# Optimization experiments

Measured on AMD Instinct MI355X. Metric: run time of the kernel, lower is better.

The kernel has to match this reference:

```python
import jax, jax.numpy as jnp
import numpy as np

B, S, D, H, DFF = 4, 2048, 1024, 16, 4096
DH = D // H  # per-head query/value dim
EPS = 1e-5


def layer_norm(x, scale, bias):
    mu = jnp.mean(x, axis=-1, keepdims=True)
    var = jnp.mean(jnp.square(x - mu), axis=-1, keepdims=True)
    return (x - mu) * jax.lax.rsqrt(var + EPS) * scale + bias


def setup_inputs() -> dict:
    key = jax.random.key(0)
    ks = jax.random.split(key, 16)
    s_in = 1.0 / np.sqrt(D)
    s_ff = 1.0 / np.sqrt(DFF)
    inp = {
        "x": jax.random.normal(ks[0], (B, S, D), jnp.float32),
        # per-head Q/K/V projections stacked along head axis [H, D, DH]
        "wq": jax.random.normal(ks[1], (H, D, DH), jnp.float32) * s_in,
        "bq": jax.random.normal(ks[2], (H, DH), jnp.float32) * 0.01,
        "wk": jax.random.normal(ks[3], (H, D, DH), jnp.float32) * s_in,
        "bk": jax.random.normal(ks[4], (H, DH), jnp.float32) * 0.01,
        "wv": jax.random.normal(ks[5], (H, D, DH), jnp.float32) * s_in,
        "bv": jax.random.normal(ks[6], (H, DH), jnp.float32) * 0.01,
        "wo": jax.random.normal(ks[7], (H * DH, D), jnp.float32) * s_in,
        "bo": jax.random.normal(ks[8], (D,), jnp.float32) * 0.01,
        "ln1_s": jnp.ones((D,), jnp.float32),
        "ln1_b": jnp.zeros((D,), jnp.float32),
        "w1": jax.random.normal(ks[9], (D, DFF), jnp.float32) * s_in,
        "b1": jax.random.normal(ks[10], (DFF,), jnp.float32) * 0.01,
        "w2": jax.random.normal(ks[11], (DFF, D), jnp.float32) * s_ff,
        "b2": jax.random.normal(ks[12], (D,), jnp.float32) * 0.01,
        "ln2_s": jnp.ones((D,), jnp.float32),
        "ln2_b": jnp.zeros((D,), jnp.float32),
    }
    return inp


def reference(x, wq, bq, wk, bk, wv, bv, wo, bo, ln1_s, ln1_b, w1, b1, w2, b2, ln2_s, ln2_b):
    # --- masked multi-head self-attention (all heads vectorized) ---
    q = jnp.einsum('bsd,hde->bhse', x, wq) + bq[None, :, None, :]  # [B,H,S,DH]
    k = jnp.einsum('bsd,hde->bhse', x, wk) + bk[None, :, None, :]
    v = jnp.einsum('bsd,hde->bhse', x, wv) + bv[None, :, None, :]
    scores = jnp.einsum('bhse,bhte->bhst', q, k)  # [B,H,S,S]
    causal = jnp.tril(jnp.ones((S, S), bool))  # mask sets strict upper triangle to -inf
    scores = jnp.where(causal, scores, -jnp.inf)
    scale = jnp.float32(DH) ** 0.5
    attn = jax.nn.softmax(scores / scale, axis=-1)
    out = jnp.einsum('bhst,bhte->bhse', attn, v)  # [B,H,S,DH]
    concat = out.transpose(0, 2, 1, 3).reshape(B, S, H * DH)
    attn_out = concat @ wo + bo
    y = layer_norm(x + attn_out, ln1_s, ln1_b)  # post-LN residual (dropout=0)
    # --- feed-forward ---
    ff = jax.nn.relu(y @ w1 + b1) @ w2 + b2
    return layer_norm(y + ff, ln2_s, ln2_b)
```

## Files before the change

kernel.cpp:

```cpp
#include <hip/hip_runtime.h>
#include <hip/hip_bf16.h>
#include <cstdint>

#define BB 4
#define SS 2048
#define DD 1024
#define HH 16
#define DHH 64
#define DFFN 4096
#define MROWS (BB*SS)

typedef __attribute__((ext_vector_type(8))) __bf16 v8bf;
typedef __attribute__((ext_vector_type(4))) float v4f;

static __device__ __forceinline__ unsigned short f2bf(float f) {
  unsigned u = __float_as_uint(f);
  u = (u + 0x7fffu + ((u >> 16) & 1u)) >> 16;
  return (unsigned short)u;
}

static __device__ __forceinline__ unsigned bf2bits(__hip_bfloat162 h) {
  union { __hip_bfloat162 h; unsigned u; } cv; cv.h = h; return cv.u;
}

static __device__ __forceinline__ void mfma16(v4f& d, v8bf a, v8bf b) {
  d = __builtin_amdgcn_mfma_f32_16x16x32_bf16(a, b, d, 0, 0, 0);
}

static __device__ __forceinline__ void gload16(const void* g, void* l) {
  __builtin_amdgcn_global_load_lds(
      (const __attribute__((address_space(1))) unsigned int*)(unsigned long long)g,
      (__attribute__((address_space(3))) unsigned int*)(unsigned int)(unsigned long long)l,
      16, 0, 0);
}

static __device__ __forceinline__ unsigned xcd_work(unsigned hw, unsigned nwg) {
  return (hw & 7u) * (nwg >> 3) + (hw >> 3);
}


__global__ __launch_bounds__(256) void pack_x_k(const float* __restrict__ x,
                                                unsigned short* __restrict__ xb) {
  int i = blockIdx.x * 256 + threadIdx.x;
  float4 v = ((const float4*)x)[i];
  ushort4 o;
  o.x = f2bf(v.x); o.y = f2bf(v.y); o.z = f2bf(v.z); o.w = f2bf(v.w);
  ((ushort4*)xb)[i] = o;
}

static __device__ __forceinline__ void transpose_tile(const float* __restrict__ src,
                                                      unsigned short* __restrict__ dst,
                                                      int R, int C, int rt, int ct) {
  __shared__ float tile[32][33];
  const int tx = threadIdx.x, ty = threadIdx.y;
  #pragma unroll
  for (int j = 0; j < 4; ++j)
    tile[ty + j * 8][tx] = src[(size_t)(rt + ty + j * 8) * C + ct + tx];
  __syncthreads();
  #pragma unroll
  for (int j = 0; j < 4; ++j)
    dst[(size_t)(ct + ty + j * 8) * R + rt + tx] = f2bf(tile[tx][ty + j * 8]);
}

__global__ __launch_bounds__(256) void transpose_k(const float* __restrict__ src,
                                                   unsigned short* __restrict__ dst,
                                                   int R, int C) {
  transpose_tile(src, dst, R, C, blockIdx.y * 32, blockIdx.x * 32);
}

__global__ __launch_bounds__(256) void transpose_qkv_k(const float* __restrict__ wq,
                                                       const float* __restrict__ wk,
                                                       const float* __restrict__ wv,
                                                       unsigned short* __restrict__ dst) {
  const int z = blockIdx.z;
  const int w = z >> 4, h = z & 15;
  const float* src = (w == 0) ? wq : ((w == 1) ? wk : wv);
  src += (size_t)h * DD * DHH;
  unsigned short* d = dst + (size_t)(w * DD + h * DHH) * DD;
  transpose_tile(src, d, DD, DHH, blockIdx.y * 32, blockIdx.x * 32);
}

template<int MODE>
static __device__ __forceinline__ void gemm_epi(
    const v4f& a4, int rb, int col, int N,
    const float* __restrict__ bias0, const float* __restrict__ bias1,
    const float* __restrict__ bias2,
    float* __restrict__ outF, unsigned short* __restrict__ o0,
    unsigned short* __restrict__ o1, unsigned short* __restrict__ o2) {
  if constexpr (MODE == 0) {
    const int seg = col >> 10, cc = col & 1023;
    const int h = cc >> 6, e = cc & 63;
    const float bias = (seg == 0) ? bias0[cc] : (seg == 1) ? bias1[cc] : bias2[cc];
    if (seg < 2) {
      unsigned short* dst = (seg == 0) ? o0 : o1;
      const float scl = (seg == 0) ? 0.18033688f : 1.0f;
      #pragma unroll
      for (int i = 0; i < 4; ++i) {
        const int row = rb + i, b = row >> 11, s = row & (SS - 1);
        dst[(((size_t)b * HH + h) * SS + s) * DHH + e] = f2bf((a4[i] + bias) * scl);
      }
    } else {
      const int b = rb >> 11, s0q = rb & (SS - 1);
      ushort4 pv;
      pv.x = f2bf(a4[0] + bias);
      pv.y = f2bf(a4[1] + bias);
      pv.z = f2bf(a4[2] + bias);
      pv.w = f2bf(a4[3] + bias);
      *(ushort4*)&o2[(((size_t)b * HH + h) * DHH + e) * SS + s0q] = pv;
    }
  } else if constexpr (MODE == 1 || MODE == 3) {
    const float bias = bias0[col];
    #pragma unroll
    for (int i = 0; i < 4; ++i)
      outF[(size_t)(rb + i) * N + col] = a4[i] + bias;
  } else {
    const float bias = bias0[col];
    #pragma unroll
    for (int i = 0; i < 4; ++i)
      o0[(size_t)(rb + i) * N + col] = f2bf(fmaxf(a4[i] + bias, 0.f));
  }
}


template<int MODE>
__global__ __launch_bounds__(512, 2) void gemm_bt(
    const unsigned short* __restrict__ A, const unsigned short* __restrict__ Bt,
    const float* __restrict__ bias0, const float* __restrict__ bias1,
    const float* __restrict__ bias2,
    float* __restrict__ outF, unsigned short* __restrict__ o0,
    unsigned short* __restrict__ o1, unsigned short* __restrict__ o2,
    int M, int N, int K) {
  extern __shared__ __align__(16) char smem[];
  const int tid = threadIdx.x;
  const int wid = tid >> 6, lane = tid & 63;
  const int l15 = lane & 15, kg = lane >> 4;
  const unsigned nwg = gridDim.x * gridDim.y;
  const unsigned work = xcd_work(blockIdx.y * gridDim.x + blockIdx.x, nwg);
  const int m0 = (int)(work / gridDim.x) * 256, n0 = (int)(work % gridDim.x) * 256;
  const int wm = (wid >> 2) * 128, wn = (wid & 3) * 64;

  const int sr8 = wid * 8 + (lane >> 3);
  const int sge = ((lane & 7) ^ ((lane >> 3) & 7)) << 3;
  const int swr = (l15 & 7) << 4;

  const int NK = K >> 6;
  v4f acc[8][4] = {};

  #define STA(q, kt, lb) gload16(A  + (size_t)(m0 + (q) * 64 + sr8) * K + (kt) * 64 + sge, \
                                 (lb) + (q) * 8192 + wid * 1024)
  #define STB(q, kt, lb) gload16(Bt + (size_t)(n0 + (q) * 64 + sr8) * K + (kt) * 64 + sge, \
                                 (lb) + (q) * 8192 + wid * 1024)

  {
    char* A0b = smem;
    char* B0b = smem + 65536;
    STB(0, 0, B0b); STB(1, 0, B0b); STB(2, 0, B0b); STB(3, 0, B0b);
    STA(0, 0, A0b); STA(2, 0, A0b); STA(1, 0, A0b); STA(3, 0, A0b);
    asm volatile("s_waitcnt vmcnt(2)" ::: "memory");
    __builtin_amdgcn_s_barrier();
  }

  #pragma unroll 1
  for (int j = 0; j < NK; ++j) {
    char* Ac = smem + (j & 1) * 32768;
    char* Bc = smem + 65536 + (j & 1) * 32768;
    char* An = smem + ((j + 1) & 1) * 32768;
    char* Bn = smem + 65536 + ((j + 1) & 1) * 32768;
    const bool more = (j + 1 < NK);

    v8bf bf_[4][2], af01[4][2];
    #pragma unroll
    for (int nr = 0; nr < 4; ++nr)
      #pragma unroll
      for (int ks = 0; ks < 2; ++ks)
        bf_[nr][ks] = *(const v8bf*)(Bc + (wn + nr * 16 + l15) * 128 +
                                     (((ks * 4 + kg) << 4) ^ swr));
    #pragma unroll
    for (int mi = 0; mi < 4; ++mi)
      #pragma unroll
      for (int ks = 0; ks < 2; ++ks)
        af01[mi][ks] = *(const v8bf*)(Ac + (wm + mi * 16 + l15) * 128 +
                                      (((ks * 4 + kg) << 4) ^ swr));
    if (more) { STB(0, j + 1, Bn); STB(1, j + 1, Bn); STB(2, j + 1, Bn); STB(3, j + 1, Bn); }
    __builtin_amdgcn_s_setprio(1);
    #pragma unroll
    for (int mi = 0; mi < 2; ++mi)
      #pragma unroll
      for (int nr = 0; nr < 4; ++nr)
        #pragma unroll
        for (int ks = 0; ks < 2; ++ks)
          mfma16(acc[mi][nr], af01[mi][ks], bf_[nr][ks]);
    __builtin_amdgcn_s_setprio(0);
    __builtin_amdgcn_s_barrier();

    if (more) {
      STA(0, j + 1, An); STA(2, j + 1, An); STA(1, j + 1, An); STA(3, j + 1, An);
      asm volatile("s_waitcnt vmcnt(8)" ::: "memory");
    } else {
      asm volatile("s_waitcnt vmcnt(0)" ::: "memory");
    }
    __builtin_amdgcn_s_setprio(1);
    #pragma unroll
    for (int mi = 2; mi < 4; ++mi)
      #pragma unroll
      for (int nr = 0; nr < 4; ++nr)
        #pragma unroll
        for (int ks = 0; ks < 2; ++ks)
          mfma16(acc[mi][nr], af01[mi][ks], bf_[nr][ks]);
    __builtin_amdgcn_s_setprio(0);
    __builtin_amdgcn_s_barrier();

    v8bf af23[4][2];
    #pragma unroll
    for (int mi = 0; mi < 4; ++mi)
      #pragma unroll
      for (int ks = 0; ks < 2; ++ks)
        af23[mi][ks] = *(const v8bf*)(Ac + (wm + (mi + 4) * 16 + l15) * 128 +
                                      (((ks * 4 + kg) << 4) ^ swr));
    __builtin_amdgcn_s_setprio(1);
    #pragma unroll
    for (int mi = 0; mi < 2; ++mi)
      #pragma unroll
      for (int nr = 0; nr < 4; ++nr)
        #pragma unroll
        for (int ks = 0; ks < 2; ++ks)
          mfma16(acc[mi + 4][nr], af23[mi][ks], bf_[nr][ks]);
    __builtin_amdgcn_s_setprio(0);
    __builtin_amdgcn_s_barrier();

    if (more) asm volatile("s_waitcnt vmcnt(2)" ::: "memory");
    __builtin_amdgcn_s_setprio(1);
    #pragma unroll
    for (int mi = 2; mi < 4; ++mi)
      #pragma unroll
      for (int nr = 0; nr < 4; ++nr)
        #pragma unroll
        for (int ks = 0; ks < 2; ++ks)
          mfma16(acc[mi + 4][nr], af23[mi][ks], bf_[nr][ks]);
    __builtin_amdgcn_s_setprio(0);
    __builtin_amdgcn_s_barrier();
  }
  #undef STA
  #undef STB

  #pragma unroll
  for (int nr = 0; nr < 4; ++nr) {
    const int col = n0 + wn + nr * 16 + l15;
    #pragma unroll
    for (int mr = 0; mr < 8; ++mr)
      gemm_epi<MODE>(acc[mr][nr], m0 + wm + mr * 16 + kg * 4, col, N,
                     bias0, bias1, bias2, outF, o0, o1, o2);
  }
}


template<int MODE>
__global__ __launch_bounds__(512, 2) void gemm_bt_n(
    const unsigned short* __restrict__ A, const unsigned short* __restrict__ Bt,
    const float* __restrict__ bias0, const float* __restrict__ bias1,
    const float* __restrict__ bias2,
    float* __restrict__ outF, unsigned short* __restrict__ o0,
    unsigned short* __restrict__ o1, unsigned short* __restrict__ o2,
    int M, int N, int K) {
  extern __shared__ __align__(16) char smem[];
  const int tid = threadIdx.x;
  const int wid = tid >> 6, lane = tid & 63;
  const int l15 = lane & 15, kg = lane >> 4;
  const unsigned nwg = gridDim.x * gridDim.y;
  const unsigned work = xcd_work(blockIdx.y * gridDim.x + blockIdx.x, nwg);
  const int m0 = (int)(work / gridDim.x) * 256, n0 = (int)(work % gridDim.x) * 128;
  const int wm = (wid >> 1) * 64, wn = (wid & 1) * 64;

  const int sr8 = wid * 8 + (lane >> 3);
  const int sge = ((lane & 7) ^ ((lane >> 3) & 7)) << 3;
  const int swr = (l15 & 7) << 4;

  const int NK = K >> 6;
  v4f acc[4][4] = {};

  #define STA(q, kt, lb) gload16(A  + (size_t)(m0 + (q) * 64 + sr8) * K + (kt) * 64 + sge, \
                                 (lb) + (q) * 8192 + wid * 1024)
  #define STB(q, kt, lb) gload16(Bt + (size_t)(n0 + (q) * 64 + sr8) * K + (kt) * 64 + sge, \
                                 (lb) + (q) * 8192 + wid * 1024)

  {
    char* A0b = smem;
    char* B0b = smem + 65536;
    STB(0, 0, B0b); STB(1, 0, B0b);
    STA(0, 0, A0b); STA(1, 0, A0b); STA(2, 0, A0b); STA(3, 0, A0b);
    asm volatile("s_waitcnt vmcnt(0)" ::: "memory");
    __builtin_amdgcn_s_barrier();
  }

  #pragma unroll 1
  for (int j = 0; j < NK; ++j) {
    char* Ac = smem + (j & 1) * 32768;
    char* Bc = smem + 65536 + (j & 1) * 16384;
    char* An = smem + ((j + 1) & 1) * 32768;
    char* Bn = smem + 65536 + ((j + 1) & 1) * 16384;
    const bool more = (j + 1 < NK);

    v8bf bf_[4][2], af01[2][2];
    #pragma unroll
    for (int nr = 0; nr < 4; ++nr)
      #pragma unroll
      for (int ks = 0; ks < 2; ++ks)
        bf_[nr][ks] = *(const v8bf*)(Bc + (wn + nr * 16 + l15) * 128 +
                                     (((ks * 4 + kg) << 4) ^ swr));
    #pragma unroll
    for (int mi = 0; mi < 2; ++mi)
      #pragma unroll
      for (int ks = 0; ks < 2; ++ks)
        af01[mi][ks] = *(const v8bf*)(Ac + (wm + mi * 16 + l15) * 128 +
                                      (((ks * 4 + kg) << 4) ^ swr));
    if (more) {
      STB(0, j + 1, Bn); STB(1, j + 1, Bn);
      STA(0, j + 1, An); STA(1, j + 1, An); STA(2, j + 1, An); STA(3, j + 1, An);
    }
    __builtin_amdgcn_s_setprio(1);
    #pragma unroll
    for (int mi = 0; mi < 2; ++mi)
      #pragma unroll
      for (int nr = 0; nr < 4; ++nr)
        #pragma unroll
        for (int ks = 0; ks < 2; ++ks)
          mfma16(acc[mi][nr], af01[mi][ks], bf_[nr][ks]);
    __builtin_amdgcn_s_setprio(0);
    __builtin_amdgcn_s_barrier();

    v8bf af23[2][2];
    #pragma unroll
    for (int mi = 0; mi < 2; ++mi)
      #pragma unroll
      for (int ks = 0; ks < 2; ++ks)
        af23[mi][ks] = *(const v8bf*)(Ac + (wm + (mi + 2) * 16 + l15) * 128 +
                                      (((ks * 4 + kg) << 4) ^ swr));
    __builtin_amdgcn_s_setprio(1);
    #pragma unroll
    for (int mi = 0; mi < 2; ++mi)
      #pragma unroll
      for (int nr = 0; nr < 4; ++nr)
        #pragma unroll
        for (int ks = 0; ks < 2; ++ks)
          mfma16(acc[mi + 2][nr], af23[mi][ks], bf_[nr][ks]);
    __builtin_amdgcn_s_setprio(0);
    if (more) asm volatile("s_waitcnt vmcnt(0)" ::: "memory");
    __builtin_amdgcn_s_barrier();
  }
  #undef STA
  #undef STB

  #pragma unroll
  for (int nr = 0; nr < 4; ++nr) {
    const int col = n0 + wn + nr * 16 + l15;
    #pragma unroll
    for (int mr = 0; mr < 4; ++mr)
      gemm_epi<MODE>(acc[mr][nr], m0 + wm + mr * 16 + kg * 4, col, N,
                     bias0, bias1, bias2, outF, o0, o1, o2);
  }
}

__global__ __launch_bounds__(512) void attn_k(const unsigned short* __restrict__ q,
                                              const unsigned short* __restrict__ k,
                                              const unsigned short* __restrict__ vt,
                                              unsigned short* __restrict__ concat) {
  __shared__ __align__(16) unsigned short Ks[64 * 64];
  __shared__ __align__(16) unsigned short Vs[64 * 64];
  __shared__ __align__(16) unsigned short PL[8][16 * 72];

  const int tid = threadIdx.x, wid = tid >> 6, lane = tid & 63;
  const int l15 = lane & 15, kg = lane >> 4;
  const unsigned work = xcd_work(blockIdx.y * 8 + blockIdx.x, 512);
  const int qxi = work & 7, bh = (int)(work >> 3);
  const int b = bh >> 4, h = bh & 15;

  const char* kb = (const char*)(k + (size_t)bh * SS * DHH);
  const char* vb = (const char*)(vt + (size_t)bh * DHH * SS);
  unsigned short* ob = concat + (size_t)b * SS * DD + h * DHH;

  const int srow = wid * 8 + (lane >> 3);
  const int swz_c = ((lane & 7) * 16) ^ ((lane >> 3) << 4);
  const int swr = (l15 & 7) << 4;
  unsigned short* pl = &PL[wid][0];

  #pragma unroll 1
  for (int half = 0; half < 2; ++half) {
    const int qt = (half == 0) ? qxi : 15 - qxi;
    const int q0 = qt * 128;
    const int q0w = q0 + wid * 16;
    const unsigned short* qb = q + ((size_t)bh * SS + q0w) * DHH;
    const int qrow = q0w + l15;

    v8bf qf[2];
    #pragma unroll
    for (int ks = 0; ks < 2; ++ks)
      qf[ks] = *(const v8bf*)&qb[l15 * DHH + ks * 32 + kg * 8];

    v4f acc[4] = {};
    float mrun = -1e30f, ssum = 0.f;

    const int T = qt * 2 + 2;
    for (int it = 0; it < T; ++it) {
      const int t0 = it * 64;
      gload16(kb + (size_t)(t0 + srow) * 128 + swz_c, &Ks[(wid * 8) * 64]);
      gload16(vb + (size_t)srow * 4096 + (size_t)t0 * 2 + swz_c, &Vs[(wid * 8) * 64]);
      __syncthreads();

      if (t0 <= q0w + 15) {
        v4f sT[4] = {};
        #pragma unroll
        for (int mt = 0; mt < 4; ++mt) {
          #pragma unroll
          for (int ks = 0; ks < 2; ++ks) {
            const v8bf kf = *(const v8bf*)((const char*)Ks + (mt * 16 + l15) * 128 +
                                           ((ks * 64 + kg * 16) ^ swr));
            mfma16(sT[mt], kf, qf[ks]);
          }
        }

        const bool full = (t0 + 63 <= q0w);
        float p[16];
        #pragma unroll
        for (int mt = 0; mt < 4; ++mt)
          #pragma unroll
          for (int rg = 0; rg < 4; ++rg) {
            float s = sT[mt][rg];
            if (!full) s = (t0 + mt * 16 + kg * 4 + rg <= qrow) ? s : -1e30f;
            p[mt * 4 + rg] = s;
          }
        float m8[8], m4_[4];
        #pragma unroll
        for (int i = 0; i < 8; ++i) m8[i] = fmaxf(p[2 * i], p[2 * i + 1]);
        #pragma unroll
        for (int i = 0; i < 4; ++i) m4_[i] = fmaxf(m8[2 * i], m8[2 * i + 1]);
        float mx = fmaxf(fmaxf(m4_[0], m4_[1]), fmaxf(m4_[2], m4_[3]));
        mx = fmaxf(mx, __shfl_xor(mx, 16));
        mx = fmaxf(mx, __shfl_xor(mx, 32));
        if (!__all(mx - mrun <= 8.0f)) {
          const float mnew = fmaxf(mrun, mx);
          const float fac = exp2f(mrun - mnew);
          mrun = mnew;
          ssum *= fac;
          #pragma unroll
          for (int mt = 0; mt < 4; ++mt) acc[mt] *= fac;
        }
        #pragma unroll
        for (int i = 0; i < 16; ++i) p[i] = exp2f(p[i] - mrun);
        float s8[8], s4_[4];
        #pragma unroll
        for (int i = 0; i < 8; ++i) s8[i] = p[2 * i] + p[2 * i + 1];
        #pragma unroll
        for (int i = 0; i < 4; ++i) s4_[i] = s8[2 * i] + s8[2 * i + 1];
        float ts = (s4_[0] + s4_[1]) + (s4_[2] + s4_[3]);
        ts += __shfl_xor(ts, 16);
        ts += __shfl_xor(ts, 32);
        ssum += ts;
        #pragma unroll
        for (int mt = 0; mt < 4; ++mt) {
          uint2 w;
          w.x = bf2bits(__float22bfloat162_rn(make_float2(p[mt * 4 + 0], p[mt * 4 + 1])));
          w.y = bf2bits(__float22bfloat162_rn(make_float2(p[mt * 4 + 2], p[mt * 4 + 3])));
          *(uint2*)((char*)pl + l15 * 144 + mt * 32 + kg * 8) = w;
        }
        asm volatile("s_waitcnt lgkmcnt(0)" ::: "memory");
        __builtin_amdgcn_sched_barrier(0);

        #pragma unroll
        for (int ks = 0; ks < 2; ++ks) {
          const v8bf pb = *(const v8bf*)((const char*)pl + l15 * 144 + ks * 64 + kg * 16);
          #pragma unroll
          for (int mt = 0; mt < 4; ++mt) {
            const v8bf va = *(const v8bf*)((const char*)Vs + (mt * 16 + l15) * 128 +
                                           ((ks * 64 + kg * 16) ^ swr));
            mfma16(acc[mt], va, pb);
          }
        }
      }
      __syncthreads();
    }

    const float inv = 1.0f / ssum;
    #pragma unroll
    for (int mt = 0; mt < 4; ++mt) {
      ushort4 o4;
      o4.x = f2bf(acc[mt][0] * inv);
      o4.y = f2bf(acc[mt][1] * inv);
      o4.z = f2bf(acc[mt][2] * inv);
      o4.w = f2bf(acc[mt][3] * inv);
      *(ushort4*)&ob[(size_t)qrow * DD + mt * 16 + kg * 4] = o4;
    }
  }
}

template<bool WB>
__global__ __launch_bounds__(256) void resid_ln_k(const float* __restrict__ a,
                                                  const float* __restrict__ t,
                                                  const float* __restrict__ sc,
                                                  const float* __restrict__ bi,
                                                  float* __restrict__ yo,
                                                  unsigned short* __restrict__ yb) {
  __shared__ float rs[4], rs2[4];
  const int row = blockIdx.x, tid = threadIdx.x;
  const int wid = tid >> 6, lane = tid & 63;
  const float4 x4 = ((const float4*)(a + (size_t)row * DD))[tid];
  const float4 t4 = ((const float4*)(t + (size_t)row * DD))[tid];
  const float v0 = x4.x + t4.x, v1 = x4.y + t4.y, v2 = x4.z + t4.z, v3 = x4.w + t4.w;
  float s = v0 + v1 + v2 + v3;
  float s2 = v0 * v0 + v1 * v1 + v2 * v2 + v3 * v3;
  #pragma unroll
  for (int m = 1; m < 64; m <<= 1) { s += __shfl_xor(s, m); s2 += __shfl_xor(s2, m); }
  if (lane == 0) { rs[wid] = s; rs2[wid] = s2; }
  __syncthreads();
  s = rs[0] + rs[1] + rs[2] + rs[3];
  s2 = rs2[0] + rs2[1] + rs2[2] + rs2[3];
  const float mu = s * (1.0f / DD);
  const float var = s2 * (1.0f / DD) - mu * mu;
  const float rstd = rsqrtf(var + 1e-5f);
  const int c0 = tid * 4;
  const float o0 = (v0 - mu) * rstd * sc[c0 + 0] + bi[c0 + 0];
  const float o1 = (v1 - mu) * rstd * sc[c0 + 1] + bi[c0 + 1];
  const float o2 = (v2 - mu) * rstd * sc[c0 + 2] + bi[c0 + 2];
  const float o3 = (v3 - mu) * rstd * sc[c0 + 3] + bi[c0 + 3];
  float4 ov; ov.x = o0; ov.y = o1; ov.z = o2; ov.w = o3;
  ((float4*)(yo + (size_t)row * DD))[tid] = ov;
  if (WB) {
    ushort4 ub; ub.x = f2bf(o0); ub.y = f2bf(o1); ub.z = f2bf(o2); ub.w = f2bf(o3);
    ((ushort4*)(yb + (size_t)row * DD))[tid] = ub;
  }
}


extern "C" void kernel_launch(void* const* d_in, const int* in_sizes, int n_in,
                              void* d_out, int out_size, void* d_ws, size_t ws_size,
                              hipStream_t stream) {
  const float* x   = (const float*)d_in[0];
  const float* wq  = (const float*)d_in[1];
  const float* bq  = (const float*)d_in[2];
  const float* wk  = (const float*)d_in[3];
  const float* bk  = (const float*)d_in[4];
  const float* wv  = (const float*)d_in[5];
  const float* bv  = (const float*)d_in[6];
  const float* wo  = (const float*)d_in[7];
  const float* bo  = (const float*)d_in[8];
  const float* l1s = (const float*)d_in[9];
  const float* l1b = (const float*)d_in[10];
  const float* w1  = (const float*)d_in[11];
  const float* b1  = (const float*)d_in[12];
  const float* w2  = (const float*)d_in[13];
  const float* b2  = (const float*)d_in[14];
  const float* l2s = (const float*)d_in[15];
  const float* l2b = (const float*)d_in[16];

  char* ws = (char*)d_ws;
  unsigned short* WO_T  = (unsigned short*)(ws + 0);
  unsigned short* W1_T  = (unsigned short*)(ws + 2097152);
  unsigned short* W2_T  = (unsigned short*)(ws + 10485760);
  float*          Y     = (float*)(ws + 18874368);
  unsigned short* YBF   = (unsigned short*)(ws + 52428800);
  float*          TMP1  = (float*)(ws + 69206016);
  unsigned short* XBF   = (unsigned short*)(ws + 102760448);
  unsigned short* WQKVT = (unsigned short*)(ws + 119537664);
  unsigned short* QB    = (unsigned short*)(ws + 125829120);
  unsigned short* KB    = (unsigned short*)(ws + 142606336);
  unsigned short* VTB   = (unsigned short*)(ws + 159383552);
  unsigned short* CONC  = (unsigned short*)(ws + 176160768);
  unsigned short* H1    = (unsigned short*)(ws + 102760448);
  float*          TMP2  = TMP1;

  constexpr int GSMEM  = 131072;
  constexpr int GSMEMN = 98304;
  hipFuncSetAttribute(reinterpret_cast<const void*>(gemm_bt<2>),
                      hipFuncAttributeMaxDynamicSharedMemorySize, GSMEM);
  hipFuncSetAttribute(reinterpret_cast<const void*>(gemm_bt_n<0>),
                      hipFuncAttributeMaxDynamicSharedMemorySize, GSMEMN);
  hipFuncSetAttribute(reinterpret_cast<const void*>(gemm_bt_n<1>),
                      hipFuncAttributeMaxDynamicSharedMemorySize, GSMEMN);
  hipFuncSetAttribute(reinterpret_cast<const void*>(gemm_bt_n<3>),
                      hipFuncAttributeMaxDynamicSharedMemorySize, GSMEMN);

  pack_x_k<<<8192, 256, 0, stream>>>(x, XBF);
  transpose_qkv_k<<<dim3(2, 32, 48), dim3(32, 8), 0, stream>>>(wq, wk, wv, WQKVT);
  transpose_k<<<dim3(32, 32),  dim3(32, 8), 0, stream>>>(wo, WO_T, 1024, 1024);
  transpose_k<<<dim3(128, 32), dim3(32, 8), 0, stream>>>(w1, W1_T, 1024, 4096);
  transpose_k<<<dim3(32, 128), dim3(32, 8), 0, stream>>>(w2, W2_T, 4096, 1024);

  gemm_bt_n<0><<<dim3(24, 32), 512, GSMEMN, stream>>>(XBF, WQKVT, bq, bk, bv,
      nullptr, QB, KB, VTB, MROWS, 3072, 1024);
  attn_k<<<dim3(8, 64), 512, 0, stream>>>(QB, KB, VTB, CONC);
  gemm_bt_n<1><<<dim3(8, 32), 512, GSMEMN, stream>>>(CONC, WO_T, bo, nullptr, nullptr,
      TMP1, nullptr, nullptr, nullptr, MROWS, 1024, 1024);
  resid_ln_k<true><<<8192, 256, 0, stream>>>(x, TMP1, l1s, l1b, Y, YBF);
  gemm_bt<2><<<dim3(16, 32), 512, GSMEM, stream>>>(YBF, W1_T, b1, nullptr, nullptr,
      nullptr, H1, nullptr, nullptr, MROWS, 4096, 1024);
  gemm_bt_n<3><<<dim3(8, 32), 512, GSMEMN, stream>>>(H1, W2_T, b2, nullptr, nullptr,
      TMP2, nullptr, nullptr, nullptr, MROWS, 1024, 4096);
  resid_ln_k<false><<<8192, 256, 0, stream>>>(Y, TMP2, l2s, l2b, (float*)d_out, nullptr);
}
```

Baseline: 394.5 us.

## Single-buffer gemm_bt LDS and raise occupancy instead of double-buffered pipeline

Replaces the double-buffered, interleaved load/MFMA schedule in gemm_bt (used for the FFN1 ReLU GEMM, MODE 2) with a single LDS buffer: wait for all loads, barrier, compute the full 64-wide K step, barrier, then issue the next tile's loads. LDS drops from 128KB to 64KB and launch bounds request 4 blocks per CU, so latency is meant to be hidden by more resident workgroups instead of in-kernel prefetch. This exposes global load latency within each block, and 512 threads × 4 blocks with a 128-float accumulator per thread may not fit the register file, so the occupancy target may not be reached or may force spills.

```diff
diff --git a/kernel.cpp b/kernel.cpp
--- a/kernel.cpp
+++ b/kernel.cpp
@@ -123,7 +123,7 @@
 
 
 template<int MODE>
-__global__ __launch_bounds__(512, 2) void gemm_bt(
+__global__ __launch_bounds__(512, 4) void gemm_bt(
     const unsigned short* __restrict__ A, const unsigned short* __restrict__ Bt,
     const float* __restrict__ bias0, const float* __restrict__ bias1,
     const float* __restrict__ bias2,
@@ -146,99 +146,47 @@
   const int NK = K >> 6;
   v4f acc[8][4] = {};
 
-  #define STA(q, kt, lb) gload16(A  + (size_t)(m0 + (q) * 64 + sr8) * K + (kt) * 64 + sge, \
-                                 (lb) + (q) * 8192 + wid * 1024)
-  #define STB(q, kt, lb) gload16(Bt + (size_t)(n0 + (q) * 64 + sr8) * K + (kt) * 64 + sge, \
-                                 (lb) + (q) * 8192 + wid * 1024)
-
-  {
-    char* A0b = smem;
-    char* B0b = smem + 65536;
-    STB(0, 0, B0b); STB(1, 0, B0b); STB(2, 0, B0b); STB(3, 0, B0b);
-    STA(0, 0, A0b); STA(2, 0, A0b); STA(1, 0, A0b); STA(3, 0, A0b);
-    asm volatile("s_waitcnt vmcnt(2)" ::: "memory");
-    __builtin_amdgcn_s_barrier();
-  }
+  #define STA(q, kt) gload16(A  + (size_t)(m0 + (q) * 64 + sr8) * K + (kt) * 64 + sge, \
+                             smem + (q) * 8192 + wid * 1024)
+  #define STB(q, kt) gload16(Bt + (size_t)(n0 + (q) * 64 + sr8) * K + (kt) * 64 + sge, \
+                             smem + 32768 + (q) * 8192 + wid * 1024)
+
+  STA(0, 0); STA(1, 0); STA(2, 0); STA(3, 0);
+  STB(0, 0); STB(1, 0); STB(2, 0); STB(3, 0);
 
   #pragma unroll 1
   for (int j = 0; j < NK; ++j) {
-    char* Ac = smem + (j & 1) * 32768;
-    char* Bc = smem + 65536 + (j & 1) * 32768;
-    char* An = smem + ((j + 1) & 1) * 32768;
-    char* Bn = smem + 65536 + ((j + 1) & 1) * 32768;
-    const bool more = (j + 1 < NK);
-
-    v8bf bf_[4][2], af01[4][2];
+    asm volatile("s_waitcnt vmcnt(0)" ::: "memory");
+    __builtin_amdgcn_s_barrier();
+
+    v8bf bf_[4][2], af[8][2];
     #pragma unroll
     for (int nr = 0; nr < 4; ++nr)
       #pragma unroll
       for (int ks = 0; ks < 2; ++ks)
-        bf_[nr][ks] = *(const v8bf*)(Bc + (wn + nr * 16 + l15) * 128 +
+        bf_[nr][ks] = *(const v8bf*)(smem + 32768 + (wn + nr * 16 + l15) * 128 +
                                      (((ks * 4 + kg) << 4) ^ swr));
     #pragma unroll
-    for (int mi = 0; mi < 4; ++mi)
+    for (int mi = 0; mi < 8; ++mi)
       #pragma unroll
       for (int ks = 0; ks < 2; ++ks)
-        af01[mi][ks] = *(const v8bf*)(Ac + (wm + mi * 16 + l15) * 128 +
-                                      (((ks * 4 + kg) << 4) ^ swr));
-    if (more) { STB(0, j + 1, Bn); STB(1, j + 1, Bn); STB(2, j + 1, Bn); STB(3, j + 1, Bn); }
+        af[mi][ks] = *(const v8bf*)(smem + (wm + mi * 16 + l15) * 128 +
+                                    (((ks * 4 + kg) << 4) ^ swr));
     __builtin_amdgcn_s_setprio(1);
     #pragma unroll
-    for (int mi = 0; mi < 2; ++mi)
+    for (int mi = 0; mi < 8; ++mi)
       #pragma unroll
       for (int nr = 0; nr < 4; ++nr)
         #pragma unroll
         for (int ks = 0; ks < 2; ++ks)
-          mfma16(acc[mi][nr], af01[mi][ks], bf_[nr][ks]);
+          mfma16(acc[mi][nr], af[mi][ks], bf_[nr][ks]);
     __builtin_amdgcn_s_setprio(0);
     __builtin_amdgcn_s_barrier();
 
-    if (more) {
-      STA(0, j + 1, An); STA(2, j + 1, An); STA(1, j + 1, An); STA(3, j + 1, An);
-      asm volatile("s_waitcnt vmcnt(8)" ::: "memory");
-    } else {
-      asm volatile("s_waitcnt vmcnt(0)" ::: "memory");
+    if (j + 1 < NK) {
+      STA(0, j + 1); STA(1, j + 1); STA(2, j + 1); STA(3, j + 1);
+      STB(0, j + 1); STB(1, j + 1); STB(2, j + 1); STB(3, j + 1);
     }
-    __builtin_amdgcn_s_setprio(1);
-    #pragma unroll
-    for (int mi = 2; mi < 4; ++mi)
-      #pragma unroll
-      for (int nr = 0; nr < 4; ++nr)
-        #pragma unroll
-        for (int ks = 0; ks < 2; ++ks)
-          mfma16(acc[mi][nr], af01[mi][ks], bf_[nr][ks]);
-    __builtin_amdgcn_s_setprio(0);
-    __builtin_amdgcn_s_barrier();
-
-    v8bf af23[4][2];
-    #pragma unroll
-    for (int mi = 0; mi < 4; ++mi)
-      #pragma unroll
-      for (int ks = 0; ks < 2; ++ks)
-        af23[mi][ks] = *(const v8bf*)(Ac + (wm + (mi + 4) * 16 + l15) * 128 +
-                                      (((ks * 4 + kg) << 4) ^ swr));
-    __builtin_amdgcn_s_setprio(1);
-    #pragma unroll
-    for (int mi = 0; mi < 2; ++mi)
-      #pragma unroll
-      for (int nr = 0; nr < 4; ++nr)
-        #pragma unroll
-        for (int ks = 0; ks < 2; ++ks)
-          mfma16(acc[mi + 4][nr], af23[mi][ks], bf_[nr][ks]);
-    __builtin_amdgcn_s_setprio(0);
-    __builtin_amdgcn_s_barrier();
-
-    if (more) asm volatile("s_waitcnt vmcnt(2)" ::: "memory");
-    __builtin_amdgcn_s_setprio(1);
-    #pragma unroll
-    for (int mi = 2; mi < 4; ++mi)
-      #pragma unroll
-      for (int nr = 0; nr < 4; ++nr)
-        #pragma unroll
-        for (int ks = 0; ks < 2; ++ks)
-          mfma16(acc[mi + 4][nr], af23[mi][ks], bf_[nr][ks]);
-    __builtin_amdgcn_s_setprio(0);
-    __builtin_amdgcn_s_barrier();
   }
   #undef STA
   #undef STB
@@ -567,7 +515,7 @@
   unsigned short* H1    = (unsigned short*)(ws + 102760448);
   float*          TMP2  = TMP1;
 
-  constexpr int GSMEM  = 131072;
+  constexpr int GSMEM  = 65536;
   constexpr int GSMEMN = 98304;
   hipFuncSetAttribute(reinterpret_cast<const void*>(gemm_bt<2>),
                       hipFuncAttributeMaxDynamicSharedMemorySize, GSMEM);
```

Result: slower. 1.304 ms (+230.5%).
